# Performance work log

Measured on AMD Instinct MI355X. Metric: run time of the kernel, lower is better.

Reference implementation:

```python
import jax, jax.numpy as jnp
import numpy as np
from jax import lax

C = 512      # channels
K = 5        # dynamic_k
NH = 8       # num_heads
HID = 32     # channels // reduction
B, Hsp, Wsp = 8, 32, 32
EPS = 1e-5


def conv2d(x, w, b, pad):
    # x [B,Cin,H,W], w [Cout,Cin,kh,kw] -> NCHW conv (cross-correlation, like torch)
    y = lax.conv_general_dilated(x, w, (1, 1), [(pad, pad), (pad, pad)],
                                 dimension_numbers=('NCHW', 'OIHW', 'NCHW'))
    return y + b[None, :, None, None]


def setup_inputs() -> dict:
    key = jax.random.key(0)
    ks = jax.random.split(key, 20)
    s = 0.02
    inp = {
        'vi_feat': jax.random.normal(ks[0], (B, C, Hsp, Wsp), jnp.float32),
        'ir_feat': jax.random.normal(ks[1], (B, C, Hsp, Wsp), jnp.float32),
        # dynamic_conv: 1x1 convs treated as dense on pooled vector
        'dc_w1': jax.random.normal(ks[2], (4 * C, C), jnp.float32) * s,
        'dc_b1': jnp.zeros((4 * C,), jnp.float32),
        'dc_w2': jax.random.normal(ks[3], (K * K, 4 * C), jnp.float32) * s,
        'dc_b2': jnp.zeros((K * K,), jnp.float32),
        # cross-attention projections (torch MultiheadAttention layout: y = x @ W.T + b)
        'Wq': jax.random.normal(ks[4], (C, C), jnp.float32) * s,
        'bq': jnp.zeros((C,), jnp.float32),
        'Wk': jax.random.normal(ks[5], (C, C), jnp.float32) * s,
        'bk': jnp.zeros((C,), jnp.float32),
        'Wv': jax.random.normal(ks[6], (C, C), jnp.float32) * s,
        'bv': jnp.zeros((C,), jnp.float32),
        'Wo': jax.random.normal(ks[7], (C, C), jnp.float32) * s,
        'bo': jnp.zeros((C,), jnp.float32),
        # gate convs
        'gate_w1': jax.random.normal(ks[8], (HID, 2 * C, 3, 3), jnp.float32) * s,
        'gate_b1': jnp.zeros((HID,), jnp.float32),
        'gate_w2': jax.random.normal(ks[9], (2, HID, 3, 3), jnp.float32) * s,
        'gate_b2': jnp.zeros((2,), jnp.float32),
        # enhance: conv3x3 + BN (inference stats) + SiLU
        'enh_w': jax.random.normal(ks[10], (C, C, 3, 3), jnp.float32) * s,
        'enh_b': jnp.zeros((C,), jnp.float32),
        'bn_gamma': jnp.ones((C,), jnp.float32),
        'bn_beta': jnp.zeros((C,), jnp.float32),
        'bn_mean': jnp.zeros((C,), jnp.float32),
        'bn_var': jnp.ones((C,), jnp.float32),
    }
    return inp


def defa_forward(vi_feat, ir_feat, dc_w1, dc_b1, dc_w2, dc_b2,
                 Wq, bq, Wk, bk, Wv, bv, Wo, bo,
                 gate_w1, gate_b1, gate_w2, gate_b2,
                 enh_w, enh_b, bn_gamma, bn_beta, bn_mean, bn_var):
    b, c, h, w = vi_feat.shape
    n = h * w
    hd = c // NH

    # ---- dynamic_conv: GAP -> 1x1 -> ReLU -> 1x1 -> softmax over k^2 ----
    pooled = (vi_feat + ir_feat).mean(axis=(2, 3))                 # [B,C]
    hid = jax.nn.relu(pooled @ dc_w1.T + dc_b1)                    # [B,4C]
    kw = jax.nn.softmax(hid @ dc_w2.T + dc_b2, axis=1)             # [B,K*K]

    # ---- cross attention: query=vi, key=value=ir ----
    vi_seq = vi_feat.reshape(b, c, n).transpose(0, 2, 1)           # [B,N,C]
    ir_seq = ir_feat.reshape(b, c, n).transpose(0, 2, 1)
    q = (vi_seq @ Wq.T + bq).reshape(b, n, NH, hd)
    k_ = (ir_seq @ Wk.T + bk).reshape(b, n, NH, hd)
    v = (ir_seq @ Wv.T + bv).reshape(b, n, NH, hd)
    scores = jnp.einsum('bqhd,bkhd->bhqk', q, k_) / jnp.sqrt(jnp.float32(hd))
    attn = jax.nn.softmax(scores, axis=-1)
    ctx = jnp.einsum('bhqk,bkhd->bqhd', attn, v).reshape(b, n, c)
    fused_seq = ctx @ Wo.T + bo                                    # [B,N,C]
    fused_feat = fused_seq.transpose(0, 2, 1).reshape(b, c, h, w)

    # ---- dynamic per-pixel conv: unfold -> weighted sum == per-sample depthwise
    # correlation with the (shared-across-channels) KxK kernel kw ----
    ker = jnp.broadcast_to(kw.reshape(b, 1, 1, K, K), (b, c, 1, K, K))

    def one_sample(f, kk):  # f [C,H,W], kk [C,1,K,K]
        y = lax.conv_general_dilated(f[None], kk, (1, 1),
                                     [(K // 2, K // 2)] * 2,
                                     dimension_numbers=('NCHW', 'OIHW', 'NCHW'),
                                     feature_group_count=c)
        return y[0]

    dynamic_feat = jax.vmap(one_sample)(fused_feat, ker)           # [B,C,H,W]

    # ---- gated fusion ----
    gates = jax.nn.sigmoid(conv2d(jax.nn.relu(conv2d(
        jnp.concatenate([vi_feat, ir_feat], axis=1), gate_w1, gate_b1, 1)),
        gate_w2, gate_b2, 1))                                      # [B,2,H,W]
    w_vi, w_ir = gates[:, 0:1], gates[:, 1:2]
    fused = (w_ir * dynamic_feat + vi_feat) + (w_vi * dynamic_feat + ir_feat)

    # ---- enhance: conv3x3 + BN(inference) + SiLU ----
    y = conv2d(fused, enh_w, enh_b, 1)
    y = (y - bn_mean[None, :, None, None]) * (bn_gamma / jnp.sqrt(bn_var + EPS))[None, :, None, None] + bn_beta[None, :, None, None]
    return y * jax.nn.sigmoid(y)


def reference(vi_feat, ir_feat, dc_w1, dc_b1, dc_w2, dc_b2,
              Wq, bq, Wk, bk, Wv, bv, Wo, bo,
              gate_w1, gate_b1, gate_w2, gate_b2,
              enh_w, enh_b, bn_gamma, bn_beta, bn_mean, bn_var):
    return defa_forward(vi_feat, ir_feat, dc_w1, dc_b1, dc_w2, dc_b2,
                        Wq, bq, Wk, bk, Wv, bv, Wo, bo,
                        gate_w1, gate_b1, gate_w2, gate_b2,
                        enh_w, enh_b, bn_gamma, bn_beta, bn_mean, bn_var)
```

## Files before the change

kernel.cpp:

```cpp
#include <hip/hip_runtime.h>

typedef __bf16 bf16;
typedef __attribute__((ext_vector_type(2))) __bf16 bf16x2;
typedef __attribute__((ext_vector_type(4))) __bf16 bf16x4;
typedef __attribute__((ext_vector_type(8))) __bf16 bf16x8;
typedef __attribute__((ext_vector_type(4))) float f32x4;

constexpr size_t OFF_CATSEQ = 0;
constexpr size_t OFF_WBF    = 16777216;
constexpr size_t OFF_ENHW   = 18874368;
constexpr size_t OFF_GW1R   = 23592960;
constexpr size_t OFF_CHS    = 24182784;
constexpr size_t OFF_ZP     = 24186880;
constexpr size_t OFF_POOL   = 24187136;
constexpr size_t OFF_HID    = 24203520;
constexpr size_t OFF_KW     = 24269056;
constexpr size_t OFF_Q      = 24270080;
constexpr size_t OFF_K      = 32658688;
constexpr size_t OFF_VT     = 41047296;
constexpr size_t OFF_CTX    = 49435904;
constexpr size_t OFF_FF     = 57824512;
constexpr size_t OFF_G1P    = 66213120;
constexpr size_t OFF_Y1     = 75650304;
constexpr size_t OFF_GSUM   = 76698880;
constexpr size_t OFF_F2     = 76731648;

struct KParams {
  const float *vi, *ir, *bq, *bk, *bv, *bo, *gb1;
  char* ws;
  float* out;
};

__device__ __forceinline__ void gload16(const void* g, void* l) {
  __builtin_amdgcn_global_load_lds(
      (const __attribute__((address_space(1))) unsigned int*)g,
      (__attribute__((address_space(3))) unsigned int*)l, 16, 0, 0);
}

template<int N> __device__ __forceinline__ void waitvm() {
  if constexpr (N==0) asm volatile("s_waitcnt vmcnt(0)" ::: "memory");
  else if constexpr (N==1) asm volatile("s_waitcnt vmcnt(1)" ::: "memory");
  else if constexpr (N==2) asm volatile("s_waitcnt vmcnt(2)" ::: "memory");
  else if constexpr (N==3) asm volatile("s_waitcnt vmcnt(3)" ::: "memory");
  else if constexpr (N==4) asm volatile("s_waitcnt vmcnt(4)" ::: "memory");
  else if constexpr (N==6) asm volatile("s_waitcnt vmcnt(6)" ::: "memory");
  else if constexpr (N==8) asm volatile("s_waitcnt vmcnt(8)" ::: "memory");
  else asm volatile("s_waitcnt vmcnt(12)" ::: "memory");
}

__global__ __launch_bounds__(256) void k_wprep(const float* Wq, const float* Wk, const float* Wv, const float* Wo,
                        const float* enh_w, const float* gw1,
                        const float* enh_b, const float* gamma, const float* beta,
                        const float* mean, const float* var,
                        bf16* wbf, bf16* enhw, bf16* gw1r, float* chs, float* zp)
{
  __shared__ float ld[9216];
  int blk = blockIdx.x, tid = threadIdx.x;
  if (blk < 4099) {
    long i = (long)blk*256 + tid;
    if (i < 1048576) {
      int which = (int)(i >> 18); long r = i & 262143;
      const float* s = which==0?Wq: which==1?Wk: which==2?Wv:Wo;
      wbf[i] = (bf16)s[r];
    } else if (i < 1048576+512) {
      int c = (int)(i - 1048576);
      float sc = gamma[c]*rsqrtf(var[c]+1e-5f);
      chs[c] = sc; chs[512+c] = (enh_b[c]-mean[c])*sc + beta[c];
    } else if (i < 1048576+512+64) {
      zp[i - (1048576+512)] = 0.f;
    }
  } else if (blk < 4099+512) {
    int co = blk - 4099;
    const float* src = enh_w + (long)co*4608;
    #pragma unroll
    for (int it=0; it<18; ++it) ld[tid + 256*it] = src[tid + 256*it];
    __syncthreads();
    #pragma unroll
    for (int t=0;t<9;++t) {
      int ci = tid*2;
      bf16x2 v = { (bf16)ld[ci*9 + t], (bf16)ld[(ci+1)*9 + t] };
      ((bf16x2*)(enhw + (long)t*262144 + (long)co*512))[tid] = v;
    }
  } else {
    int hid = blk - (4099+512);
    const float* src = gw1 + (long)hid*9216;
    #pragma unroll
    for (int it=0; it<36; ++it) ld[tid + 256*it] = src[tid + 256*it];
    __syncthreads();
    #pragma unroll
    for (int t=0;t<9;++t) {
      int ci = tid*4;
      bf16x4 v = { (bf16)ld[ci*9+t], (bf16)ld[(ci+1)*9+t],
                   (bf16)ld[(ci+2)*9+t], (bf16)ld[(ci+3)*9+t] };
      *(bf16x4*)(gw1r + (long)t*32768 + (long)hid*1024 + ci) = v;
    }
  }
}

__global__ __launch_bounds__(256) void k_cat(const float* vi, const float* ir, bf16* cat)
{
  __shared__ float ld[32][129];
  int pt = blockIdx.x, ct = blockIdx.y, b = blockIdx.z;
  const float* src = (ct < 16) ? vi : ir;
  int c0 = (ct & 15) * 32;
  int tid = threadIdx.x;
  int p0 = pt * 128;
  for (int it = 0; it < 4; ++it) {
    int row = it*8 + (tid>>5);
    int pc  = (tid & 31) * 4;
    float4 v = *(const float4*)(src + ((long)(b*512 + c0 + row))*1024 + p0 + pc);
    ld[row][pc+0]=v.x; ld[row][pc+1]=v.y; ld[row][pc+2]=v.z; ld[row][pc+3]=v.w;
  }
  __syncthreads();
  int p = tid >> 1, half = tid & 1;
  bf16x8 o0, o1;
  #pragma unroll
  for (int j = 0; j < 8; ++j) o0[j] = (bf16)ld[half*16 + j][p];
  #pragma unroll
  for (int j = 0; j < 8; ++j) o1[j] = (bf16)ld[half*16 + 8 + j][p];
  long ccol = (ct<16 ? 0 : 512) + c0 + half*16;
  bf16* dst = cat + ((long)(b*1024 + p0 + p))*1024 + ccol;
  *(bf16x8*)dst       = o0;
  *((bf16x8*)dst + 1) = o1;
}

__global__ __launch_bounds__(256) void k_poolp(const bf16* cat, float* partial)
{
  int blk = blockIdx.x; int b = blk>>3, pt = blk&7;
  int tid = threadIdx.x;
  const bf16* base = cat + ((long)(b*1024) + pt*128)*1024;
  float a0=0,a1=0,a2=0,a3=0;
  for (int p=0; p<128; ++p) {
    bf16x4 v1 = *(const bf16x4*)(base + (long)p*1024 + tid*4);
    bf16x4 v2 = *(const bf16x4*)(base + (long)p*1024 + 512 + tid*4);
    a0 += (float)v1[0] + (float)v2[0];
    a1 += (float)v1[1] + (float)v2[1];
    a2 += (float)v1[2] + (float)v2[2];
    a3 += (float)v1[3] + (float)v2[3];
  }
  float4 o = {a0,a1,a2,a3};
  *(float4*)(partial + ((long)(b*8+pt))*512 + tid*4) = o;
}

__global__ __launch_bounds__(256) void k_mlp1(const float* partial, const float* w1, const float* b1, float* hid)
{
  __shared__ float pl[8*512];
  int tid = threadIdx.x;
  const float4* pp4 = (const float4*)partial;
  #pragma unroll
  for (int k=0;k<4;++k) {
    int j = tid + 256*k;
    int b = j>>7, c4 = j&127;
    float4 s = {0,0,0,0};
    #pragma unroll
    for (int pt=0;pt<8;++pt) {
      float4 v = pp4[(b*8+pt)*128 + c4];
      s.x+=v.x; s.y+=v.y; s.z+=v.z; s.w+=v.w;
    }
    float4 o = {s.x*(1.f/1024.f), s.y*(1.f/1024.f), s.z*(1.f/1024.f), s.w*(1.f/1024.f)};
    ((float4*)pl)[j] = o;
  }
  __syncthreads();
  int lane = tid&63, wave = tid>>6;
  #pragma unroll
  for (int rr=0; rr<4; ++rr) {
    int row = (blockIdx.x*4 + wave)*4 + rr;
    const float* wr = w1 + (long)row*512;
    float acc[8] = {};
    #pragma unroll
    for (int e=0;e<8;++e) {
      int c = lane + 64*e;
      float w = wr[c];
      #pragma unroll
      for (int b=0;b<8;++b) acc[b] += w * pl[b*512+c];
    }
    #pragma unroll
    for (int b=0;b<8;++b) {
      float s = acc[b];
      #pragma unroll
      for (int off=32; off; off>>=1) s += __shfl_down(s, off);
      if (lane==0) hid[b*2048 + row] = fmaxf(s + b1[row], 0.f);
    }
  }
}

__global__ __launch_bounds__(256) void k_mlp2a(const float* hid, const float* w2, const float* b2, float* lg)
{
  int blk = blockIdx.x; int b = blk/25, j = blk%25;
  int tid = threadIdx.x, lane = tid&63, wave = tid>>6;
  const float4* h4 = (const float4*)(hid + b*2048);
  const float4* w4 = (const float4*)(w2 + (long)j*2048);
  float4 a0 = h4[tid*2], a1 = h4[tid*2+1];
  float4 c0 = w4[tid*2], c1 = w4[tid*2+1];
  float s = a0.x*c0.x+a0.y*c0.y+a0.z*c0.z+a0.w*c0.w
          + a1.x*c1.x+a1.y*c1.y+a1.z*c1.z+a1.w*c1.w;
  #pragma unroll
  for (int off=32; off; off>>=1) s += __shfl_down(s, off);
  __shared__ float wsum[4];
  if (lane==0) wsum[wave] = s;
  __syncthreads();
  if (tid==0) lg[b*25+j] = wsum[0]+wsum[1]+wsum[2]+wsum[3] + b2[j];
}

__global__ __launch_bounds__(64) void k_smax(const float* lg, float* kw)
{
  int b = threadIdx.x;
  if (b < 8) {
    float mx = -1e30f;
    for (int j=0;j<25;++j) mx = fmaxf(mx, lg[b*25+j]);
    float e[25], s = 0.f;
    for (int j=0;j<25;++j){ e[j]=__expf(lg[b*25+j]-mx); s+=e[j]; }
    float inv = 1.f/s;
    for (int j=0;j<25;++j) kw[b*32+j] = e[j]*inv;
  }
}

template<int OP, int BM, int BN, int WAVES_M, int KSTEPS>
__global__ __launch_bounds__(256)
void k_gemm(KParams p)
{
  constexpr int WAVES_N = 4/WAVES_M;
  constexpr int MT = BM/(WAVES_M*16);
  constexpr int NT = BN/(WAVES_N*16);
  constexpr int ACH = (BM*4 + 255)/256;
  constexpr int BCH = (BN*4 + 255)/256;
  constexpr int WAITN = (BM*4)/256 + BCH;
  __shared__ bf16 As[3][BM*32];
  __shared__ bf16 Bs[3][BN*32];
  const int tid = threadIdx.x, lane = tid&63, wave = tid>>6;
  const int g = lane>>4, l15 = lane&15;
  const int wm = wave % WAVES_M, wn = wave / WAVES_M;

  int b, which = 0, tapc = 0, kg = 0, m0, n0;
  const bf16 *Aptr, *Bptr;
  long ldb, lda;
  const int wg = blockIdx.x;
  if constexpr (OP==0) {
    b = wg&7; which = wg>>8;
    int xy = (wg>>3)&31;
    m0 = (xy>>3)*BM; n0 = (xy&7)*BN;
    Aptr = (const bf16*)(p.ws+OFF_WBF) + (long)which*262144;
    Bptr = (const bf16*)(p.ws+OFF_CATSEQ) + (long)b*1048576 + (which?512:0);
    ldb = 1024; lda = 512;
  } else if constexpr (OP==1) {
    b = wg&7;
    int xy = wg>>3;
    m0 = (xy>>3)*BM; n0 = (xy&7)*BN;
    Aptr = (const bf16*)(p.ws+OFF_WBF) + 3L*262144;
    Bptr = (const bf16*)(p.ws+OFF_CTX) + (long)b*524288;
    ldb = 512; lda = 512;
  } else if constexpr (OP==2) {
    b = wg&7;
    int loc = wg>>3;
    kg = loc>>5;
    int xy = loc&31;
    m0 = (xy>>3)*BM; n0 = (xy&7)*BN;
    Aptr = (const bf16*)(p.ws+OFF_ENHW);
    Bptr = (const bf16*)(p.ws+OFF_F2) + (long)b*524288;
    ldb = 512; lda = 512;
  } else {
    b = wg&7;
    int loc = wg>>3;
    tapc = loc>>3;
    m0 = 0; n0 = (loc&7)*BN;
    Aptr = (const bf16*)(p.ws+OFF_GW1R) + (long)tapc*32768;
    Bptr = (const bf16*)(p.ws+OFF_CATSEQ) + (long)b*1048576;
    ldb = 1024; lda = 1024;
  }
  const bf16* zp = (const bf16*)(p.ws+OFF_ZP);

  int tap = (OP==2) ? (kg*72)>>4 : tapc;
  int kcc = (OP==2) ? (kg*72)&15 : 0;
  const bf16* pA[ACH];
  const bf16* pB[BCH];
  bool aact[ACH];
  bool bval[BCH];
  int bpp[BCH], bss8[BCH];
  int dstA[ACH], dstB[BCH];
  #pragma unroll
  for (int i=0;i<ACH;++i) {
    int cc_ = tid + 256*i;
    aact[i] = cc_ < BM*4;
    int c = aact[i] ? cc_ : 0;
    int row = c>>2, slot = c&3, ss = slot ^ ((row>>1)&3);
    dstA[i] = ((c-lane))*8;
    if constexpr (OP==2) pA[i] = Aptr + (long)tap*262144 + (long)(m0+row)*lda + kcc*32 + ss*8;
    else                 pA[i] = Aptr + (long)(m0+row)*lda + ss*8;
  }
  #pragma unroll
  for (int i=0;i<BCH;++i) {
    int c = tid + 256*i;
    int row = c>>2, slot = c&3, ss = slot ^ ((row>>1)&3);
    dstB[i] = ((c-lane))*8;
    bss8[i] = ss*8;
    if constexpr (OP==2 || OP==3) {
      int pp = n0 + row; bpp[i] = pp;
      int hh = (pp>>5) + tap/3 - 1, ww = (pp&31) + tap%3 - 1;
      bool v = ((unsigned)hh < 32u) && ((unsigned)ww < 32u);
      bval[i] = v;
      pB[i] = v ? (Bptr + (long)(hh*32+ww)*ldb + kcc*32 + ss*8) : zp;
    } else {
      bval[i] = true;
      pB[i] = Bptr + (long)(n0+row)*ldb + ss*8;
    }
  }

  auto STAGE = [&](int buf) {
    #pragma unroll
    for (int i=0;i<ACH;++i) if (aact[i]) gload16(pA[i], As[buf] + dstA[i]);
    #pragma unroll
    for (int i=0;i<BCH;++i) gload16(pB[i], Bs[buf] + dstB[i]);
  };
  auto ADV = [&]() {
    if constexpr (OP==2) {
      ++kcc;
      if (kcc == 16) {
        kcc = 0; ++tap;
        int t3 = tap/3, tm = tap%3;
        #pragma unroll
        for (int i=0;i<ACH;++i) pA[i] += 262144 - 480;
        #pragma unroll
        for (int i=0;i<BCH;++i) {
          int hh = (bpp[i]>>5) + t3 - 1, ww = (bpp[i]&31) + tm - 1;
          bool v = ((unsigned)hh < 32u) && ((unsigned)ww < 32u);
          bval[i] = v;
          pB[i] = v ? (Bptr + (long)(hh*32+ww)*ldb + bss8[i]) : zp;
        }
      } else {
        #pragma unroll
        for (int i=0;i<ACH;++i) pA[i] += 32;
        #pragma unroll
        for (int i=0;i<BCH;++i) pB[i] += bval[i] ? 32 : 0;
      }
    } else if constexpr (OP==3) {
      #pragma unroll
      for (int i=0;i<ACH;++i) pA[i] += 32;
      #pragma unroll
      for (int i=0;i<BCH;++i) pB[i] += bval[i] ? 32 : 0;
    } else {
      #pragma unroll
      for (int i=0;i<ACH;++i) pA[i] += 32;
      #pragma unroll
      for (int i=0;i<BCH;++i) pB[i] += 32;
    }
  };

  f32x4 acc[MT][NT] = {};

  STAGE(0); ADV();
  STAGE(1); ADV();
  int cur = 0, stg = 2;
  for (int ks = 0; ks < KSTEPS; ++ks) {
    if (ks+2 < KSTEPS)      { STAGE(stg); ADV(); stg = (stg==2)?0:stg+1; waitvm<2*WAITN>(); }
    else if (ks+1 < KSTEPS) { waitvm<WAITN>(); }
    else                    { waitvm<0>(); }
    __builtin_amdgcn_s_barrier();
    __builtin_amdgcn_sched_barrier(0);
    bf16x8 af[MT], bq_[NT];
    #pragma unroll
    for (int mt=0; mt<MT; ++mt) {
      int row = wm*MT*16 + mt*16 + l15;
      af[mt] = *(const bf16x8*)&As[cur][row*32 + 8*(g ^ ((row>>1)&3))];
    }
    #pragma unroll
    for (int nt=0; nt<NT; ++nt) {
      int row = wn*NT*16 + nt*16 + l15;
      bq_[nt] = *(const bf16x8*)&Bs[cur][row*32 + 8*(g ^ ((row>>1)&3))];
    }
    __builtin_amdgcn_s_setprio(1);
    #pragma unroll
    for (int mt=0; mt<MT; ++mt)
      #pragma unroll
      for (int nt=0; nt<NT; ++nt)
        acc[mt][nt] = __builtin_amdgcn_mfma_f32_16x16x32_bf16(af[mt], bq_[nt], acc[mt][nt], 0,0,0);
    __builtin_amdgcn_s_setprio(0);
    __builtin_amdgcn_s_barrier();
    cur = (cur==2)?0:cur+1;
  }

  #pragma unroll
  for (int mt=0; mt<MT; ++mt) {
    #pragma unroll
    for (int nt=0; nt<NT; ++nt) {
      #pragma unroll
      for (int reg=0; reg<4; ++reg) {
        int m = m0 + wm*MT*16 + mt*16 + 4*g + reg;
        int n = n0 + wn*NT*16 + nt*16 + l15;
        float v = acc[mt][nt][reg];
        if constexpr (OP==0) {
          const float* bias = which==0?p.bq: which==1?p.bk:p.bv;
          v += bias[m];
          if (which==0) v *= 0.18033688011112042f;
          int h = m>>6, d = m&63;
          if (which==2) ((bf16*)(p.ws+OFF_VT))[((long)(b*8+h)*64 + d)*1024 + n] = (bf16)v;
          else {
            bf16* dst = (bf16*)(p.ws + (which==0?OFF_Q:OFF_K));
            dst[((long)(b*8+h)*1024 + n)*64 + d] = (bf16)v;
          }
        } else if constexpr (OP==1) {
          v += p.bo[m];
          ((bf16*)(p.ws+OFF_FF))[((long)(b*512+m))*1024 + n] = (bf16)v;
        } else if constexpr (OP==2) {
          float* part = (float*)(p.ws+OFF_Q) + (long)kg*4194304;
          part[((long)b*512+m)*1024 + n] = v;
        } else {
          ((float*)(p.ws+OFF_G1P))[((long)((tapc*8+b)*32+m))*1024 + n] = v;
        }
      }
    }
  }
}

__global__ __launch_bounds__(256) void k_enhred(KParams p)
{
  long e = ((long)blockIdx.x*256 + threadIdx.x)*4;
  const float* part = (const float*)(p.ws+OFF_Q);
  float4 a = *(const float4*)(part + e);
  float4 c = *(const float4*)(part + 4194304 + e);
  int m = (int)((e>>10)&511);
  const float* chs = (const float*)(p.ws+OFF_CHS);
  float sc = chs[m], sh = chs[512+m];
  float4 o;
  float y0 = (a.x+c.x)*sc+sh, y1 = (a.y+c.y)*sc+sh, y2 = (a.z+c.z)*sc+sh, y3 = (a.w+c.w)*sc+sh;
  o.x = y0/(1.f+__expf(-y0)); o.y = y1/(1.f+__expf(-y1));
  o.z = y2/(1.f+__expf(-y2)); o.w = y3/(1.f+__expf(-y3));
  *(float4*)(p.out + e) = o;
}

__global__ __launch_bounds__(256)
void k_attn(KParams p)
{
  const bf16* Q = (const bf16*)(p.ws+OFF_Q);
  const bf16* K = (const bf16*)(p.ws+OFF_K);
  const bf16* V = (const bf16*)(p.ws+OFF_VT);
  bf16* ctx = (bf16*)(p.ws+OFF_CTX);
  constexpr float TH = 11.5424f;
  int wg = blockIdx.x;
  int bh = (wg&7)*8 + (wg>>7);
  int qt = (wg>>3)&15;
  int b = bh>>3, h = bh&7;
  int tid = threadIdx.x, lane = tid&63, wave = tid>>6, g = lane>>4, l15 = lane&15;
  __shared__ bf16 Ks[2][64*64];
  __shared__ bf16 Vs[2][64*64];
  __shared__ bf16 Ps[4][16*64];
  const bf16* Qw = Q + ((long)bh*1024 + qt*64 + wave*16)*64;
  bf16x8 qf[2];
  qf[0] = *(const bf16x8*)(Qw + l15*64 + g*8);
  qf[1] = *(const bf16x8*)(Qw + l15*64 + 32 + g*8);
  const bf16* Kb = K + (long)bh*65536;
  const bf16* Vb = V + (long)bh*65536;
  float mr[4] = {-1e30f,-1e30f,-1e30f,-1e30f};
  float lrp[4] = {0,0,0,0};
  f32x4 cacc[4] = {};

  const bf16* pK[2]; const bf16* pV[2];
  int dstK[2], dstV[2];
  {
    int c = tid;
    int krow = c>>3, kslot = c&7, kss = kslot ^ (krow&7);
    pK[0] = Kb + (long)krow*64 + kss*8;
    pK[1] = Kb + (long)(krow+32)*64 + (kslot ^ ((krow+32)&7))*8;
    int d = c>>3, ss2 = kslot ^ (d&7);
    pV[0] = Vb + (long)d*1024 + ss2*8;
    pV[1] = Vb + (long)(d+32)*1024 + ss2*8;
    dstK[0] = (tid-lane)*8;       dstK[1] = (tid-lane+256)*8;
    dstV[0] = (tid-lane)*8;       dstV[1] = (tid-lane+256)*8;
  }
  auto STAGE = [&](int buf) {
    gload16(pK[0], Ks[buf] + dstK[0]);
    gload16(pK[1], Ks[buf] + dstK[1]);
    gload16(pV[0], Vs[buf] + dstV[0]);
    gload16(pV[1], Vs[buf] + dstV[1]);
  };
  auto ADV = [&]() {
    pK[0] += 4096; pK[1] += 4096;
    pV[0] += 64;   pV[1] += 64;
  };

  STAGE(0); ADV();
  int cur = 0;
  for (int step = 0; step < 16; ++step) {
    if (step < 15) { STAGE(cur^1); ADV(); waitvm<4>(); }
    else           { waitvm<0>(); }
    __builtin_amdgcn_s_barrier();
    __builtin_amdgcn_sched_barrier(0);
    f32x4 s0 = {}, s1 = {}, s2 = {}, s3 = {};
    __builtin_amdgcn_s_setprio(1);
    {
      int r0 = l15, r1 = 16+l15, r2 = 32+l15, r3 = 48+l15;
      #pragma unroll
      for (int ks2=0; ks2<2; ++ks2) {
        bf16x8 kf0 = *(const bf16x8*)&Ks[cur][r0*64 + 8*((4*ks2+g)^(r0&7))];
        bf16x8 kf1 = *(const bf16x8*)&Ks[cur][r1*64 + 8*((4*ks2+g)^(r1&7))];
        bf16x8 kf2 = *(const bf16x8*)&Ks[cur][r2*64 + 8*((4*ks2+g)^(r2&7))];
        bf16x8 kf3 = *(const bf16x8*)&Ks[cur][r3*64 + 8*((4*ks2+g)^(r3&7))];
        s0 = __builtin_amdgcn_mfma_f32_16x16x32_bf16(qf[ks2], kf0, s0, 0,0,0);
        s1 = __builtin_amdgcn_mfma_f32_16x16x32_bf16(qf[ks2], kf1, s1, 0,0,0);
        s2 = __builtin_amdgcn_mfma_f32_16x16x32_bf16(qf[ks2], kf2, s2, 0,0,0);
        s3 = __builtin_amdgcn_mfma_f32_16x16x32_bf16(qf[ks2], kf3, s3, 0,0,0);
      }
    }
    __builtin_amdgcn_s_setprio(0);
    float xm[4];
    #pragma unroll
    for (int r=0;r<4;++r)
      xm[r] = fmaxf(fmaxf(s0[r],s1[r]), fmaxf(s2[r],s3[r]));
    bool need = (xm[0] > mr[0]+TH) | (xm[1] > mr[1]+TH) |
                (xm[2] > mr[2]+TH) | (xm[3] > mr[3]+TH);
    if (__any(need)) {
      #pragma unroll
      for (int r=0;r<4;++r) {
        float x = xm[r];
        x = fmaxf(x, __shfl_xor(x, 1));
        x = fmaxf(x, __shfl_xor(x, 2));
        x = fmaxf(x, __shfl_xor(x, 4));
        x = fmaxf(x, __shfl_xor(x, 8));
        float mn = fmaxf(mr[r], x);
        float al = __builtin_amdgcn_exp2f(mr[r]-mn);
        mr[r] = mn; lrp[r] *= al;
        cacc[0][r]*=al; cacc[1][r]*=al; cacc[2][r]*=al; cacc[3][r]*=al;
      }
    }
    bf16* Pw = Ps[wave];
    #pragma unroll
    for (int r=0;r<4;++r) {
      float p0 = __builtin_amdgcn_exp2f(s0[r]-mr[r]);
      float p1 = __builtin_amdgcn_exp2f(s1[r]-mr[r]);
      float p2 = __builtin_amdgcn_exp2f(s2[r]-mr[r]);
      float p3 = __builtin_amdgcn_exp2f(s3[r]-mr[r]);
      int q = 4*g + r;
      int xr = 8*(q&7);
      Pw[q*64 + ((     l15) ^ xr)] = (bf16)p0;
      Pw[q*64 + ((16 + l15) ^ xr)] = (bf16)p1;
      Pw[q*64 + ((32 + l15) ^ xr)] = (bf16)p2;
      Pw[q*64 + ((48 + l15) ^ xr)] = (bf16)p3;
      lrp[r] += (p0+p1)+(p2+p3);
    }
    bf16x8 pa0 = *(const bf16x8*)&Pw[l15*64 + 8*((  g)^(l15&7))];
    bf16x8 pa1 = *(const bf16x8*)&Pw[l15*64 + 8*((4+g)^(l15&7))];
    __builtin_amdgcn_s_setprio(1);
    #pragma unroll
    for (int nt=0;nt<4;++nt) {
      int d = nt*16 + l15;
      bf16x8 vf0 = *(const bf16x8*)&Vs[cur][d*64 + 8*((  g)^(d&7))];
      bf16x8 vf1 = *(const bf16x8*)&Vs[cur][d*64 + 8*((4+g)^(d&7))];
      cacc[nt] = __builtin_amdgcn_mfma_f32_16x16x32_bf16(pa0, vf0, cacc[nt], 0,0,0);
      cacc[nt] = __builtin_amdgcn_mfma_f32_16x16x32_bf16(pa1, vf1, cacc[nt], 0,0,0);
    }
    __builtin_amdgcn_s_setprio(0);
    __builtin_amdgcn_s_barrier();
    cur ^= 1;
  }
  float lr[4];
  #pragma unroll
  for (int r=0;r<4;++r) {
    float s = lrp[r];
    s += __shfl_xor(s, 1);
    s += __shfl_xor(s, 2);
    s += __shfl_xor(s, 4);
    s += __shfl_xor(s, 8);
    lr[r] = s;
  }
  #pragma unroll
  for (int nt=0;nt<4;++nt) {
    #pragma unroll
    for (int r=0;r<4;++r) {
      int q = qt*64 + wave*16 + 4*g + r;
      int cc = h*64 + nt*16 + l15;
      ctx[((long)(b*1024+q))*512 + cc] = (bf16)(cacc[nt][r] / lr[r]);
    }
  }
}

__global__ __launch_bounds__(256) void k_g1red(KParams p)
{
  long o = (long)blockIdx.x*256 + threadIdx.x;
  const float* part = (const float*)(p.ws+OFF_G1P);
  int m = (int)((o >> 10) & 31);
  float a = p.gb1[m];
  #pragma unroll
  for (int t=0;t<9;++t) a += part[(long)t*262144 + o];
  ((float*)(p.ws+OFF_Y1))[o] = fmaxf(a, 0.f);
}

__global__ __launch_bounds__(256)
void k_g2(KParams p, const float* gw2, const float* gb2)
{
  __shared__ float st[3*32*32];
  __shared__ float sg[2][32];
  int h = blockIdx.x, b = blockIdx.y;
  const float* y1 = (const float*)(p.ws+OFF_Y1) + (long)b*32768;
  int tid = threadIdx.x;
  for (int c = tid; c < 768; c += 256) {
    int e = c*4;
    int hr = e>>10, hid = (e>>5)&31, w = e&31;
    int hh = h + hr - 1;
    float4 v = {0,0,0,0};
    if ((unsigned)hh < 32u) v = *(const float4*)(y1 + hid*1024 + hh*32 + w);
    *(float4*)&st[e] = v;
  }
  __syncthreads();
  if (tid < 64) {
    int gg = tid>>5, w = tid&31;
    float acc = gb2[gg];
    for (int hid=0; hid<32; ++hid) {
      #pragma unroll
      for (int u=0;u<3;++u) {
        #pragma unroll
        for (int v=0;v<3;++v) {
          int ww = w + v - 1;
          if ((unsigned)ww < 32u)
            acc += st[(u*32+hid)*32 + ww] * gw2[((gg*32+hid)*3+u)*3+v];
        }
      }
    }
    sg[gg][w] = 1.f/(1.f+__expf(-acc));
  }
  __syncthreads();
  if (tid < 32) ((float*)(p.ws+OFF_GSUM))[b*1024 + h*32 + tid] = sg[0][tid]+sg[1][tid];
}

__global__ __launch_bounds__(512)
void k_dyn(KParams p)
{
  __shared__ float ffs[16*1024];
  int ct = blockIdx.x;
  int b  = blockIdx.y;
  int c0 = ct*16;
  int t = threadIdx.x;
  const bf16* ffg = (const bf16*)(p.ws+OFF_FF) + ((long)(b*512 + c0))*1024;
  #pragma unroll
  for (int k2 = 0; k2 < 4; ++k2) {
    int chunk = t + 512*k2;
    int c = chunk >> 7, j = chunk & 127;
    bf16x8 v = *(const bf16x8*)(ffg + (long)c*1024 + j*8);
    float* d = ffs + c*1024 + j*8;
    #pragma unroll
    for (int e=0;e<8;++e) d[e] = (float)v[e];
  }
  const float* kwp = (const float*)(p.ws+OFF_KW) + b*32;
  float kk[25];
  #pragma unroll
  for (int j=0;j<25;++j) kk[j] = kwp[j];
  __syncthreads();
  int w = t & 31;
  int h0 = t >> 5;
  #pragma unroll
  for (int pass=0; pass<2; ++pass) {
    int h = h0 + pass*16;
    int pos = h*32 + w;
    float gsw = ((const float*)(p.ws+OFF_GSUM))[b*1024 + pos];
    const bf16* cs = (const bf16*)(p.ws+OFF_CATSEQ) + ((long)(b*1024) + pos)*1024 + c0;
    bf16x8 vv0 = *(const bf16x8*)cs;
    bf16x8 vv1 = *(const bf16x8*)(cs + 8);
    bf16x8 rr0 = *(const bf16x8*)(cs + 512);
    bf16x8 rr1 = *(const bf16x8*)(cs + 520);
    bf16 outv[16];
    #pragma unroll
    for (int c=0;c<16;++c) {
      float dyn = 0.f;
      #pragma unroll
      for (int u=0;u<5;++u) {
        int hh = h+u-2;
        bool okh = (unsigned)hh < 32u;
        #pragma unroll
        for (int v=0;v<5;++v) {
          int ww = w+v-2;
          bool ok = okh && ((unsigned)ww < 32u);
          float fv = ffs[c*1024 + (hh&31)*32 + (ww&31)];
          dyn += (ok ? fv : 0.f) * kk[u*5+v];
        }
      }
      float resid = (c < 8) ? ((float)vv0[c] + (float)rr0[c])
                            : ((float)vv1[c-8] + (float)rr1[c-8]);
      float val = gsw*dyn + resid;
      outv[c] = (bf16)val;
    }
    bf16* f2 = (bf16*)(p.ws+OFF_F2) + ((long)(b*1024 + pos))*512 + c0;
    *(bf16x8*)f2       = *(bf16x8*)&outv[0];
    *((bf16x8*)f2 + 1) = *(bf16x8*)&outv[8];
  }
}

extern "C" void kernel_launch(void* const* d_in, const int* in_sizes, int n_in,
                              void* d_out, int out_size, void* d_ws, size_t ws_size,
                              hipStream_t stream)
{
  char* ws = (char*)d_ws;
  KParams p;
  p.vi = (const float*)d_in[0];  p.ir = (const float*)d_in[1];
  p.bq = (const float*)d_in[7];  p.bk = (const float*)d_in[9];
  p.bv = (const float*)d_in[11]; p.bo = (const float*)d_in[13];
  p.gb1 = (const float*)d_in[15];
  p.ws = ws; p.out = (float*)d_out;

  k_wprep<<<4643,256,0,stream>>>((const float*)d_in[6],(const float*)d_in[8],(const float*)d_in[10],(const float*)d_in[12],
      (const float*)d_in[18],(const float*)d_in[14],
      (const float*)d_in[19],(const float*)d_in[20],(const float*)d_in[21],(const float*)d_in[22],(const float*)d_in[23],
      (bf16*)(ws+OFF_WBF),(bf16*)(ws+OFF_ENHW),(bf16*)(ws+OFF_GW1R),(float*)(ws+OFF_CHS),(float*)(ws+OFF_ZP));
  k_cat<<<dim3(8,32,8),256,0,stream>>>(p.vi, p.ir, (bf16*)(ws+OFF_CATSEQ));
  k_poolp<<<64,256,0,stream>>>((const bf16*)(ws+OFF_CATSEQ),(float*)(ws+OFF_Y1));
  k_mlp1<<<128,256,0,stream>>>((const float*)(ws+OFF_Y1),(const float*)d_in[2],(const float*)d_in[3],(float*)(ws+OFF_HID));
  k_mlp2a<<<200,256,0,stream>>>((const float*)(ws+OFF_HID),(const float*)d_in[4],(const float*)d_in[5],(float*)(ws+OFF_G1P));
  k_smax<<<1,64,0,stream>>>((const float*)(ws+OFF_G1P),(float*)(ws+OFF_KW));
  k_gemm<0,128,128,2,16><<<768,256,0,stream>>>(p);
  k_attn<<<1024,256,0,stream>>>(p);
  k_gemm<1,64,128,2,16><<<512,256,0,stream>>>(p);
  k_gemm<3,32,128,1,32><<<576,256,0,stream>>>(p);
  k_g1red<<<1024,256,0,stream>>>(p);
  k_g2<<<dim3(32,8),256,0,stream>>>(p,(const float*)d_in[16],(const float*)d_in[17]);
  k_dyn<<<dim3(32,8),512,0,stream>>>(p);
  k_gemm<2,128,128,2,72><<<512,256,0,stream>>>(p);
  k_enhred<<<4096,256,0,stream>>>(p);
}
```

Baseline: 260.4 us.

## Add K-unrolled double-buffered GEMM path for enhance conv and vectorize QK stores

```diff
diff --git a/kernel.cpp b/kernel.cpp
--- a/kernel.cpp
+++ b/kernel.cpp
@@ -215,7 +215,7 @@
   }
 }
 
-template<int OP, int BM, int BN, int WAVES_M, int KSTEPS>
+template<int OP, int BM, int BN, int WAVES_M, int KSTEPS, int KU>
 __global__ __launch_bounds__(256)
 void k_gemm(KParams p)
 {
@@ -224,9 +224,10 @@
   constexpr int NT = BN/(WAVES_N*16);
   constexpr int ACH = (BM*4 + 255)/256;
   constexpr int BCH = (BN*4 + 255)/256;
-  constexpr int WAITN = (BM*4)/256 + BCH;
-  __shared__ bf16 As[3][BM*32];
-  __shared__ bf16 Bs[3][BN*32];
+  constexpr int WPS = KU*((BM*4)/256 + BCH);
+  constexpr int NBUF = (KU==2) ? 2 : 3;
+  __shared__ bf16 As[NBUF][KU*BM*32];
+  __shared__ bf16 Bs[NBUF][KU*BN*32];
   const int tid = threadIdx.x, lane = tid&63, wave = tid>>6;
   const int g = lane>>4, l15 = lane&15;
   const int wm = wave % WAVES_M, wn = wave / WAVES_M;
@@ -305,12 +306,6 @@
     }
   }
 
-  auto STAGE = [&](int buf) {
-    #pragma unroll
-    for (int i=0;i<ACH;++i) if (aact[i]) gload16(pA[i], As[buf] + dstA[i]);
-    #pragma unroll
-    for (int i=0;i<BCH;++i) gload16(pB[i], Bs[buf] + dstB[i]);
-  };
   auto ADV = [&]() {
     if constexpr (OP==2) {
       ++kcc;
@@ -345,66 +340,110 @@
     }
   };
 
+  auto STAGE = [&](int buf) {
+    #pragma unroll
+    for (int u=0;u<KU;++u) {
+      #pragma unroll
+      for (int i=0;i<ACH;++i) if (aact[i]) gload16(pA[i], As[buf] + u*BM*32 + dstA[i]);
+      #pragma unroll
+      for (int i=0;i<BCH;++i) gload16(pB[i], Bs[buf] + u*BN*32 + dstB[i]);
+      ADV();
+    }
+  };
+
   f32x4 acc[MT][NT] = {};
 
-  STAGE(0); ADV();
-  STAGE(1); ADV();
-  int cur = 0, stg = 2;
-  for (int ks = 0; ks < KSTEPS; ++ks) {
-    if (ks+2 < KSTEPS)      { STAGE(stg); ADV(); stg = (stg==2)?0:stg+1; waitvm<2*WAITN>(); }
-    else if (ks+1 < KSTEPS) { waitvm<WAITN>(); }
-    else                    { waitvm<0>(); }
-    __builtin_amdgcn_s_barrier();
-    __builtin_amdgcn_sched_barrier(0);
-    bf16x8 af[MT], bq_[NT];
-    #pragma unroll
-    for (int mt=0; mt<MT; ++mt) {
-      int row = wm*MT*16 + mt*16 + l15;
-      af[mt] = *(const bf16x8*)&As[cur][row*32 + 8*(g ^ ((row>>1)&3))];
-    }
+  auto COMPUTE = [&](int cur) {
+    #pragma unroll
+    for (int u=0;u<KU;++u) {
+      bf16x8 af[MT], bq_[NT];
+      #pragma unroll
+      for (int mt=0; mt<MT; ++mt) {
+        int row = wm*MT*16 + mt*16 + l15;
+        af[mt] = *(const bf16x8*)&As[cur][u*BM*32 + row*32 + 8*(g ^ ((row>>1)&3))];
+      }
+      #pragma unroll
+      for (int nt=0; nt<NT; ++nt) {
+        int row = wn*NT*16 + nt*16 + l15;
+        bq_[nt] = *(const bf16x8*)&Bs[cur][u*BN*32 + row*32 + 8*(g ^ ((row>>1)&3))];
+      }
+      __builtin_amdgcn_s_setprio(1);
+      #pragma unroll
+      for (int mt=0; mt<MT; ++mt)
+        #pragma unroll
+        for (int nt=0; nt<NT; ++nt)
+          acc[mt][nt] = __builtin_amdgcn_mfma_f32_16x16x32_bf16(af[mt], bq_[nt], acc[mt][nt], 0,0,0);
+      __builtin_amdgcn_s_setprio(0);
+    }
+  };
+
+  if constexpr (KU==2) {
+    STAGE(0);
+    int cur = 0;
+    for (int ks = 0; ks < KSTEPS; ++ks) {
+      if (ks+1 < KSTEPS) { STAGE(cur^1); waitvm<WPS>(); }
+      else               { waitvm<0>(); }
+      __builtin_amdgcn_s_barrier();
+      __builtin_amdgcn_sched_barrier(0);
+      COMPUTE(cur);
+      __builtin_amdgcn_s_barrier();
+      cur ^= 1;
+    }
+  } else {
+    STAGE(0);
+    STAGE(1);
+    int cur = 0, stg = 2;
+    for (int ks = 0; ks < KSTEPS; ++ks) {
+      if (ks+2 < KSTEPS)      { STAGE(stg); stg = (stg==2)?0:stg+1; waitvm<2*WPS>(); }
+      else if (ks+1 < KSTEPS) { waitvm<WPS>(); }
+      else                    { waitvm<0>(); }
+      __builtin_amdgcn_s_barrier();
+      __builtin_amdgcn_sched_barrier(0);
+      COMPUTE(cur);
+      __builtin_amdgcn_s_barrier();
+      cur = (cur==2)?0:cur+1;
+    }
+  }
+
+  #pragma unroll
+  for (int mt=0; mt<MT; ++mt) {
     #pragma unroll
     for (int nt=0; nt<NT; ++nt) {
-      int row = wn*NT*16 + nt*16 + l15;
-      bq_[nt] = *(const bf16x8*)&Bs[cur][row*32 + 8*(g ^ ((row>>1)&3))];
-    }
-    __builtin_amdgcn_s_setprio(1);
-    #pragma unroll
-    for (int mt=0; mt<MT; ++mt)
-      #pragma unroll
-      for (int nt=0; nt<NT; ++nt)
-        acc[mt][nt] = __builtin_amdgcn_mfma_f32_16x16x32_bf16(af[mt], bq_[nt], acc[mt][nt], 0,0,0);
-    __builtin_amdgcn_s_setprio(0);
-    __builtin_amdgcn_s_barrier();
-    cur = (cur==2)?0:cur+1;
-  }
-
-  #pragma unroll
-  for (int mt=0; mt<MT; ++mt) {
-    #pragma unroll
-    for (int nt=0; nt<NT; ++nt) {
-      #pragma unroll
-      for (int reg=0; reg<4; ++reg) {
-        int m = m0 + wm*MT*16 + mt*16 + 4*g + reg;
-        int n = n0 + wn*NT*16 + nt*16 + l15;
-        float v = acc[mt][nt][reg];
-        if constexpr (OP==0) {
-          const float* bias = which==0?p.bq: which==1?p.bk:p.bv;
-          v += bias[m];
+      int mb = m0 + wm*MT*16 + mt*16 + 4*g;
+      int n = n0 + wn*NT*16 + nt*16 + l15;
+      if constexpr (OP==0) {
+        const float* bias = which==0?p.bq: which==1?p.bk:p.bv;
+        float v4[4];
+        #pragma unroll
+        for (int reg=0; reg<4; ++reg) {
+          float v = acc[mt][nt][reg] + bias[mb+reg];
           if (which==0) v *= 0.18033688011112042f;
-          int h = m>>6, d = m&63;
-          if (which==2) ((bf16*)(p.ws+OFF_VT))[((long)(b*8+h)*64 + d)*1024 + n] = (bf16)v;
-          else {
-            bf16* dst = (bf16*)(p.ws + (which==0?OFF_Q:OFF_K));
-            dst[((long)(b*8+h)*1024 + n)*64 + d] = (bf16)v;
+          v4[reg] = v;
+        }
+        int h = mb>>6, d0 = mb&63;
+        if (which==2) {
+          #pragma unroll
+          for (int reg=0; reg<4; ++reg)
+            ((bf16*)(p.ws+OFF_VT))[((long)(b*8+h)*64 + d0+reg)*1024 + n] = (bf16)v4[reg];
+        } else {
+          bf16* dst = (bf16*)(p.ws + (which==0?OFF_Q:OFF_K));
+          bf16x4 o = {(bf16)v4[0],(bf16)v4[1],(bf16)v4[2],(bf16)v4[3]};
+          *(bf16x4*)(dst + ((long)(b*8+h)*1024 + n)*64 + d0) = o;
+        }
+      } else {
+        #pragma unroll
+        for (int reg=0; reg<4; ++reg) {
+          int m = mb + reg;
+          float v = acc[mt][nt][reg];
+          if constexpr (OP==1) {
+            v += p.bo[m];
+            ((bf16*)(p.ws+OFF_FF))[((long)(b*512+m))*1024 + n] = (bf16)v;
+          } else if constexpr (OP==2) {
+            float* part = (float*)(p.ws+OFF_Q) + (long)kg*4194304;
+            part[((long)b*512+m)*1024 + n] = v;
+          } else {
+            ((float*)(p.ws+OFF_G1P))[((long)((tapc*8+b)*32+m))*1024 + n] = v;
           }
-        } else if constexpr (OP==1) {
-          v += p.bo[m];
-          ((bf16*)(p.ws+OFF_FF))[((long)(b*512+m))*1024 + n] = (bf16)v;
-        } else if constexpr (OP==2) {
-          float* part = (float*)(p.ws+OFF_Q) + (long)kg*4194304;
-          part[((long)b*512+m)*1024 + n] = v;
-        } else {
-          ((float*)(p.ws+OFF_G1P))[((long)((tapc*8+b)*32+m))*1024 + n] = v;
         }
       }
     }
@@ -703,13 +742,13 @@
   k_mlp1<<<128,256,0,stream>>>((const float*)(ws+OFF_Y1),(const float*)d_in[2],(const float*)d_in[3],(float*)(ws+OFF_HID));
   k_mlp2a<<<200,256,0,stream>>>((const float*)(ws+OFF_HID),(const float*)d_in[4],(const float*)d_in[5],(float*)(ws+OFF_G1P));
   k_smax<<<1,64,0,stream>>>((const float*)(ws+OFF_G1P),(float*)(ws+OFF_KW));
-  k_gemm<0,128,128,2,16><<<768,256,0,stream>>>(p);
+  k_gemm<0,128,128,2,16,1><<<768,256,0,stream>>>(p);
   k_attn<<<1024,256,0,stream>>>(p);
-  k_gemm<1,64,128,2,16><<<512,256,0,stream>>>(p);
-  k_gemm<3,32,128,1,32><<<576,256,0,stream>>>(p);
+  k_gemm<1,64,128,2,16,1><<<512,256,0,stream>>>(p);
+  k_gemm<3,32,128,1,32,1><<<576,256,0,stream>>>(p);
   k_g1red<<<1024,256,0,stream>>>(p);
   k_g2<<<dim3(32,8),256,0,stream>>>(p,(const float*)d_in[16],(const float*)d_in[17]);
   k_dyn<<<dim3(32,8),512,0,stream>>>(p);
-  k_gemm<2,128,128,2,72><<<512,256,0,stream>>>(p);
+  k_gemm<2,128,128,2,36,2><<<512,256,0,stream>>>(p);
   k_enhred<<<4096,256,0,stream>>>(p);
 }
```

Measured after the change: 244.7 us. -6.0%, faster.
